# Optimization experiments

Measured on AMD Instinct MI355X. Metric: run time of the kernel, lower is better.

Reference implementation:

```python
import jax, jax.numpy as jnp
import numpy as np

B, NQ, NKV, D = 2, 2048, 2048, 1024
N_HEADS = 16
D_H = D // N_HEADS


def setup_inputs() -> dict:
    key = jax.random.key(0)
    ks = jax.random.split(key, 10)
    s = 0.02  # weight init scale
    return {
        "q": jax.random.normal(ks[0], (B, NQ, D), jnp.float32),
        "kv": jax.random.normal(ks[1], (B, NKV, D), jnp.float32),
        "Wq": jax.random.normal(ks[2], (D, D), jnp.float32) * s,
        "bq": jnp.zeros((D,), jnp.float32),
        "Wk": jax.random.normal(ks[3], (D, D), jnp.float32) * s,
        "bk": jnp.zeros((D,), jnp.float32),
        "Wv": jax.random.normal(ks[4], (D, D), jnp.float32) * s,
        "bv": jnp.zeros((D,), jnp.float32),
        "Wo": jax.random.normal(ks[5], (D, D), jnp.float32) * s,
        "bo": jnp.zeros((D,), jnp.float32),
    }


def reference(q, kv, Wq, bq, Wk, bk, Wv, bv, Wo, bo):
    # Linear projections (torch Linear: x @ W.T + b)
    qh = q @ Wq.T + bq   # [B, NQ, D]
    kh = kv @ Wk.T + bk  # [B, NKV, D]
    vh = kv @ Wv.T + bv  # [B, NKV, D]
    # Split heads: [B, N, H, d_h]
    qh = qh.reshape(B, NQ, N_HEADS, D_H)
    kh = kh.reshape(B, NKV, N_HEADS, D_H)
    vh = vh.reshape(B, NKV, N_HEADS, D_H)
    scale = 1.0 / jnp.sqrt(jnp.asarray(D_H, qh.dtype))
    # QK^T per head: [B, H, NQ, NKV]
    scores = jnp.einsum("bqhd,bkhd->bhqk", qh, kh) * scale
    att = jax.nn.softmax(scores, axis=-1)
    # dropout p=0.0 -> identity
    out = jnp.einsum("bhqk,bkhd->bqhd", att, vh)  # [B, NQ, H, d_h]
    out = out.reshape(B, NQ, D)
    return out @ Wo.T + bo
```

## Files before the change

kernel.cpp:

```cpp
#include <hip/hip_runtime.h>
#include <cstddef>
#include <cstdint>

using half4v  = __attribute__((ext_vector_type(4))) _Float16;
using half8   = __attribute__((ext_vector_type(8))) _Float16;
using floatx4 = __attribute__((ext_vector_type(4))) float;

#define B_   2
#define NQ_  2048
#define DM   1024
#define NH_  16
#define DH_  64
#define NTILES 32

__device__ __forceinline__ void async16(const _Float16* g, _Float16* l) {
    __builtin_amdgcn_global_load_lds(
        (const __attribute__((address_space(1))) unsigned int*)g,
        (__attribute__((address_space(3))) unsigned int*)l, 16, 0, 0);
}

__global__ __launch_bounds__(256) void cvt_all(
        const float* __restrict__ q,  const float* __restrict__ kv,
        const float* __restrict__ wq, const float* __restrict__ wk,
        const float* __restrict__ wv, const float* __restrict__ wo,
        _Float16* __restrict__ dq,  _Float16* __restrict__ dkv,
        _Float16* __restrict__ dwq, _Float16* __restrict__ dwk,
        _Float16* __restrict__ dwv, _Float16* __restrict__ dwo) {
    int blk = blockIdx.x;
    const float* s;
    _Float16* d;
    int base;
    if (blk < 2048)      { s = q;  d = dq;  base = blk; }
    else if (blk < 4096) { s = kv; d = dkv; base = blk - 2048; }
    else if (blk < 4608) { s = wq; d = dwq; base = blk - 4096; }
    else if (blk < 5120) { s = wk; d = dwk; base = blk - 4608; }
    else if (blk < 5632) { s = wv; d = dwv; base = blk - 5120; }
    else                 { s = wo; d = dwo; base = blk - 5632; }
    int i = base * 256 + threadIdx.x;
    const float4* s4 = (const float4*)s;
    float4 a = s4[2 * i], b = s4[2 * i + 1];
    half8 h;
    h[0] = (_Float16)a.x; h[1] = (_Float16)a.y; h[2] = (_Float16)a.z; h[3] = (_Float16)a.w;
    h[4] = (_Float16)b.x; h[5] = (_Float16)b.y; h[6] = (_Float16)b.z; h[7] = (_Float16)b.w;
    ((half8*)d)[i] = h;
}

__global__ __launch_bounds__(256, 3) void proj_qkv(
        const _Float16* __restrict__ q16, const _Float16* __restrict__ kv16,
        const _Float16* __restrict__ wqp, const _Float16* __restrict__ wkp,
        const _Float16* __restrict__ wvp,
        const float* __restrict__ bqp, const float* __restrict__ bkp,
        const float* __restrict__ bvp,
        _Float16* __restrict__ qh, _Float16* __restrict__ kh,
        _Float16* __restrict__ vt) {
    __shared__ _Float16 As[128 * 64];
    __shared__ _Float16 Bs[128 * 64];

    const int which = blockIdx.x >> 8;
    const int sub = blockIdx.x & 255;
    const _Float16* A = (which == 0) ? q16 : kv16;
    const _Float16* W = (which == 0) ? wqp : (which == 1) ? wkp : wvp;
    const float* bias = (which == 0) ? bqp : (which == 1) ? bkp : bvp;

    const int t = threadIdx.x;
    const int w = t >> 6, lane = t & 63;
    const int r16 = lane & 15, quad = lane >> 4;
    const int bm = (sub & 7) * 4 + ((sub >> 3) & 3);
    const int bn = sub >> 5;
    const int m0 = bm * 128, n0 = bn * 128;
    const int wm = w >> 1, wn = w & 1;

    floatx4 acc[4][4];
#pragma unroll
    for (int i = 0; i < 4; i++)
#pragma unroll
        for (int j = 0; j < 4; j++)
#pragma unroll
            for (int r = 0; r < 4; r++) acc[i][j][r] = 0.f;

    const int ph0 = quad ^ (r16 & 7), ph1 = ph0 ^ 4;

    for (int k0 = 0; k0 < DM; k0 += 64) {
        __syncthreads();
#pragma unroll
        for (int i = 0; i < 4; i++) {
            int P = i * 256 + t;
            int m = P >> 3, c = (P & 7) ^ (m & 7);
            async16(A + (size_t)(m0 + m) * DM + k0 + c * 8, &As[P * 8]);
            async16(W + (size_t)(n0 + m) * DM + k0 + c * 8, &Bs[P * 8]);
        }
        asm volatile("s_waitcnt vmcnt(0)" ::: "memory");
        __syncthreads();

        half8 af[4][2], bf[4][2];
#pragma unroll
        for (int mi = 0; mi < 4; mi++) {
            int m = wm * 64 + mi * 16 + r16;
            af[mi][0] = ((const half8*)As)[m * 8 + ph0];
            af[mi][1] = ((const half8*)As)[m * 8 + ph1];
        }
#pragma unroll
        for (int ni = 0; ni < 4; ni++) {
            int n = wn * 64 + ni * 16 + r16;
            bf[ni][0] = ((const half8*)Bs)[n * 8 + ph0];
            bf[ni][1] = ((const half8*)Bs)[n * 8 + ph1];
        }
#pragma unroll
        for (int kd = 0; kd < 2; kd++)
#pragma unroll
            for (int mi = 0; mi < 4; mi++)
#pragma unroll
                for (int ni = 0; ni < 4; ni++)
                    acc[mi][ni] = __builtin_amdgcn_mfma_f32_16x16x32_f16(
                        af[mi][kd], bf[ni][kd], acc[mi][ni], 0, 0, 0);
    }

    if (which < 2) {
        _Float16* C = (which == 0) ? qh : kh;
        const float esc = (which == 0) ? 0.125f : 1.0f;
#pragma unroll
        for (int mi = 0; mi < 4; mi++)
#pragma unroll
            for (int r = 0; r < 4; r++) {
                int row = m0 + wm * 64 + mi * 16 + quad * 4 + r;
#pragma unroll
                for (int ni = 0; ni < 4; ni++) {
                    int col = n0 + wn * 64 + ni * 16 + r16;
                    C[(size_t)row * DM + col] = (_Float16)((acc[mi][ni][r] + bias[col]) * esc);
                }
            }
    } else {
#pragma unroll
        for (int mi = 0; mi < 4; mi++) {
            int krow = m0 + wm * 64 + mi * 16 + quad * 4;
            int bb = krow >> 11, kk = krow & 2047;
#pragma unroll
            for (int ni = 0; ni < 4; ni++) {
                int col = n0 + wn * 64 + ni * 16 + r16;
                int hh = col >> 6, dd = col & 63;
                float bv = bias[col];
                half4v pk;
#pragma unroll
                for (int r = 0; r < 4; r++) pk[r] = (_Float16)(acc[mi][ni][r] + bv);
                *(half4v*)&vt[((size_t)((bb * NH_ + hh) * DH_ + dd)) * NQ_ + kk] = pk;
            }
        }
    }
}

__global__ __launch_bounds__(256, 4) void attn_mfma(const _Float16* __restrict__ Qg,
                                                    const _Float16* __restrict__ Kg,
                                                    const _Float16* __restrict__ Vt,
                                                    _Float16* __restrict__ Og) {
    __shared__ _Float16 Ps[64 * 64];
    __shared__ _Float16 Ks[2][64 * 64];
    __shared__ _Float16 Vs[2][64 * 64];

    const int t = threadIdx.x, w = t >> 6, lane = t & 63;
    const int r16 = lane & 15, quad = lane >> 4;
    const int blk = blockIdx.x;
    const int bh = (blk & 7) * 4 + ((blk >> 3) & 3);
    const int qt = blk >> 5;
    const int b = bh >> 4, h = bh & 15;

    const _Float16* qbase = Qg + (size_t)(b * NQ_ + qt * 64) * DM + h * DH_;
    const _Float16* kbase = Kg + (size_t)(b * NQ_) * DM + h * DH_;
    const _Float16* vbase = Vt + (size_t)bh * DH_ * NQ_;

#pragma unroll
    for (int i = 0; i < 2; i++) {
        int P = i * 256 + t;
        int m = P >> 3, c = (P & 7) ^ (m & 7);
        async16(qbase + (size_t)m * DM + c * 8, &Ps[P * 8]);
        async16(kbase + (size_t)m * DM + c * 8, &Ks[0][P * 8]);
        async16(vbase + (size_t)m * NQ_ + c * 8, &Vs[0][P * 8]);
    }
    asm volatile("s_waitcnt vmcnt(0)" ::: "memory");
    __syncthreads();

    const int ph0 = quad ^ (r16 & 7), ph1 = ph0 ^ 4;
    half8 Qf[2];
    {
        int m = w * 16 + r16;
        Qf[0] = ((const half8*)Ps)[m * 8 + ph0];
        Qf[1] = ((const half8*)Ps)[m * 8 + ph1];
    }

    floatx4 oaccT[4];
    float lacc = 0.f;
#pragma unroll
    for (int nd = 0; nd < 4; nd++)
#pragma unroll
        for (int r = 0; r < 4; r++) oaccT[nd][r] = 0.f;

    for (int kt = 0; kt < NTILES; kt++) {
        const int cur = kt & 1;
        asm volatile("s_waitcnt vmcnt(0)" ::: "memory");
        __syncthreads();

        if (kt + 1 < NTILES) {
            const int nxt = cur ^ 1;
#pragma unroll
            for (int i = 0; i < 2; i++) {
                int P = i * 256 + t;
                int m = P >> 3, c = (P & 7) ^ (m & 7);
                async16(kbase + (size_t)((kt + 1) * 64 + m) * DM + c * 8, &Ks[nxt][P * 8]);
                async16(vbase + (size_t)m * NQ_ + (kt + 1) * 64 + c * 8, &Vs[nxt][P * 8]);
            }
        }

        floatx4 sacc[4];
#pragma unroll
        for (int nk = 0; nk < 4; nk++)
#pragma unroll
            for (int r = 0; r < 4; r++) sacc[nk][r] = 0.f;
#pragma unroll
        for (int kd = 0; kd < 2; kd++)
#pragma unroll
            for (int nk = 0; nk < 4; nk++) {
                half8 kf = ((const half8*)Ks[cur])[(nk * 16 + r16) * 8 + (kd ? ph1 : ph0)];
                sacc[nk] = __builtin_amdgcn_mfma_f32_16x16x32_f16(kf, Qf[kd], sacc[nk], 0, 0, 0);
            }

        const int q = w * 16 + r16;
#pragma unroll
        for (int nk = 0; nk < 4; nk++) {
            float p0 = __expf(sacc[nk][0]);
            float p1 = __expf(sacc[nk][1]);
            float p2 = __expf(sacc[nk][2]);
            float p3 = __expf(sacc[nk][3]);
            lacc += (p0 + p1) + (p2 + p3);
            half4v pk;
            pk[0] = (_Float16)p0; pk[1] = (_Float16)p1;
            pk[2] = (_Float16)p2; pk[3] = (_Float16)p3;
            int phys = (nk * 2 + (quad >> 1)) ^ (r16 & 7);
            *(half4v*)&Ps[q * 64 + phys * 8 + (quad & 1) * 4] = pk;
        }

#pragma unroll
        for (int ks = 0; ks < 2; ks++) {
            half8 pf = ((const half8*)Ps)[q * 8 + ((ks * 4 + quad) ^ (r16 & 7))];
#pragma unroll
            for (int nd = 0; nd < 4; nd++) {
                half8 vf = ((const half8*)Vs[cur])[(nd * 16 + r16) * 8 + ((ks * 4 + quad) ^ (r16 & 7))];
                oaccT[nd] = __builtin_amdgcn_mfma_f32_16x16x32_f16(vf, pf, oaccT[nd], 0, 0, 0);
            }
        }
    }

    {
        float l = lacc;
        l += __shfl_xor(l, 16);
        l += __shfl_xor(l, 32);
        float inv = 1.f / l;
        int qrow = b * NQ_ + qt * 64 + w * 16 + r16;
#pragma unroll
        for (int nd = 0; nd < 4; nd++) {
            half4v o;
#pragma unroll
            for (int r = 0; r < 4; r++) o[r] = (_Float16)(oaccT[nd][r] * inv);
            *(half4v*)&Og[(size_t)qrow * DM + h * DH_ + nd * 16 + quad * 4] = o;
        }
    }
}

__global__ __launch_bounds__(256, 4) void gemm_o(const _Float16* __restrict__ A,
                                                 const _Float16* __restrict__ W,
                                                 const float* __restrict__ bias,
                                                 float* __restrict__ C) {
    __shared__ _Float16 As[64 * 64];
    __shared__ _Float16 Bs[64 * 64];

    const int t = threadIdx.x;
    const int w = t >> 6, lane = t & 63;
    const int r16 = lane & 15, quad = lane >> 4;
    const int blk = blockIdx.x;
    const int bm = (blk & 7) * 8 + ((blk >> 3) & 7);
    const int bn = blk >> 6;
    const int m0 = bm * 64, n0 = bn * 64;
    const int wm = w >> 1, wn = w & 1;

    floatx4 acc[2][2];
#pragma unroll
    for (int i = 0; i < 2; i++)
#pragma unroll
        for (int j = 0; j < 2; j++)
#pragma unroll
            for (int r = 0; r < 4; r++) acc[i][j][r] = 0.f;

    const int ph0 = quad ^ (r16 & 7), ph1 = ph0 ^ 4;

    for (int k0 = 0; k0 < DM; k0 += 64) {
        __syncthreads();
#pragma unroll
        for (int i = 0; i < 2; i++) {
            int P = i * 256 + t;
            int m = P >> 3, c = (P & 7) ^ (m & 7);
            async16(A + (size_t)(m0 + m) * DM + k0 + c * 8, &As[P * 8]);
            async16(W + (size_t)(n0 + m) * DM + k0 + c * 8, &Bs[P * 8]);
        }
        asm volatile("s_waitcnt vmcnt(0)" ::: "memory");
        __syncthreads();

        half8 af[2][2], bf[2][2];
#pragma unroll
        for (int mi = 0; mi < 2; mi++) {
            int m = wm * 32 + mi * 16 + r16;
            af[mi][0] = ((const half8*)As)[m * 8 + ph0];
            af[mi][1] = ((const half8*)As)[m * 8 + ph1];
        }
#pragma unroll
        for (int ni = 0; ni < 2; ni++) {
            int n = wn * 32 + ni * 16 + r16;
            bf[ni][0] = ((const half8*)Bs)[n * 8 + ph0];
            bf[ni][1] = ((const half8*)Bs)[n * 8 + ph1];
        }
#pragma unroll
        for (int kd = 0; kd < 2; kd++)
#pragma unroll
            for (int mi = 0; mi < 2; mi++)
#pragma unroll
                for (int ni = 0; ni < 2; ni++)
                    acc[mi][ni] = __builtin_amdgcn_mfma_f32_16x16x32_f16(
                        af[mi][kd], bf[ni][kd], acc[mi][ni], 0, 0, 0);
    }

#pragma unroll
    for (int mi = 0; mi < 2; mi++)
#pragma unroll
        for (int r = 0; r < 4; r++) {
            int row = m0 + wm * 32 + mi * 16 + quad * 4 + r;
#pragma unroll
            for (int ni = 0; ni < 2; ni++) {
                int col = n0 + wn * 32 + ni * 16 + r16;
                C[(size_t)row * DM + col] = acc[mi][ni][r] + bias[col];
            }
        }
}

extern "C" void kernel_launch(void* const* d_in, const int* in_sizes, int n_in,
                              void* d_out, int out_size, void* d_ws, size_t ws_size,
                              hipStream_t stream) {
    const float* q  = (const float*)d_in[0];
    const float* kv = (const float*)d_in[1];
    const float* Wq = (const float*)d_in[2];
    const float* bq = (const float*)d_in[3];
    const float* Wk = (const float*)d_in[4];
    const float* bk = (const float*)d_in[5];
    const float* Wv = (const float*)d_in[6];
    const float* bv = (const float*)d_in[7];
    const float* Wo = (const float*)d_in[8];
    const float* bo = (const float*)d_in[9];

    char* ws = (char*)d_ws;
    _Float16* q16  = (_Float16*)(ws);
    _Float16* kv16 = (_Float16*)(ws + (size_t)(8  << 20));
    _Float16* w16q = (_Float16*)(ws + (size_t)(16 << 20));
    _Float16* w16k = (_Float16*)(ws + (size_t)(18 << 20));
    _Float16* w16v = (_Float16*)(ws + (size_t)(20 << 20));
    _Float16* w16o = (_Float16*)(ws + (size_t)(22 << 20));
    _Float16* qh16 = (_Float16*)(ws + (size_t)(24 << 20));
    _Float16* kh16 = (_Float16*)(ws + (size_t)(32 << 20));
    _Float16* vt16 = (_Float16*)(ws + (size_t)(40 << 20));
    _Float16* ao16 = (_Float16*)(ws + (size_t)(48 << 20));

    cvt_all<<<6144, 256, 0, stream>>>(q, kv, Wq, Wk, Wv, Wo,
                                      q16, kv16, w16q, w16k, w16v, w16o);

    proj_qkv<<<768, 256, 0, stream>>>(q16, kv16, w16q, w16k, w16v,
                                      bq, bk, bv, qh16, kh16, vt16);

    attn_mfma<<<1024, 256, 0, stream>>>(qh16, kh16, vt16, ao16);

    gemm_o<<<1024, 256, 0, stream>>>(ao16, w16o, bo, (float*)d_out);
}
```

Baseline: 200.5 us.

## Rework attention to 32x32x16 MFMA with 128-row Q tiles and register-resident P

The attention kernel now gives each block 128 query rows instead of 64, so every K/V tile loaded into LDS feeds twice as many queries, and the grid is halved. Matrix ops move from 16x16x32 to 32x32x16 MFMA. The probability tile is handed to the PV product through lane shuffles instead of an LDS write/read, and s_setprio brackets the MFMA sections. In exchange, per-thread register use rises (two 16-wide output accumulators plus a 16-wide score accumulator), which may lower occupancy, and the smaller grid gives fewer blocks to hide latency.

Result: no change. 199.6 us (-0.4%).

```diff
diff --git a/kernel.cpp b/kernel.cpp
--- a/kernel.cpp
+++ b/kernel.cpp
@@ -2,9 +2,10 @@
 #include <cstddef>
 #include <cstdint>
 
-using half4v  = __attribute__((ext_vector_type(4))) _Float16;
-using half8   = __attribute__((ext_vector_type(8))) _Float16;
-using floatx4 = __attribute__((ext_vector_type(4))) float;
+using half4v   = __attribute__((ext_vector_type(4))) _Float16;
+using half8    = __attribute__((ext_vector_type(8))) _Float16;
+using floatx4  = __attribute__((ext_vector_type(4))) float;
+using floatx16 = __attribute__((ext_vector_type(16))) float;
 
 #define B_   2
 #define NQ_  2048
@@ -17,6 +18,12 @@
     __builtin_amdgcn_global_load_lds(
         (const __attribute__((address_space(1))) unsigned int*)g,
         (__attribute__((address_space(3))) unsigned int*)l, 16, 0, 0);
+}
+
+__device__ __forceinline__ unsigned pkh(float a, float b) {
+    union { _Float16 h[2]; unsigned u; } x;
+    x.h[0] = (_Float16)a; x.h[1] = (_Float16)b;
+    return x.u;
 }
 
 __global__ __launch_bounds__(256) void cvt_all(
@@ -152,46 +159,49 @@
                                                     const _Float16* __restrict__ Kg,
                                                     const _Float16* __restrict__ Vt,
                                                     _Float16* __restrict__ Og) {
-    __shared__ _Float16 Ps[64 * 64];
+    __shared__ _Float16 Qs[128 * 64];
     __shared__ _Float16 Ks[2][64 * 64];
     __shared__ _Float16 Vs[2][64 * 64];
 
     const int t = threadIdx.x, w = t >> 6, lane = t & 63;
-    const int r16 = lane & 15, quad = lane >> 4;
+    const int l31 = lane & 31, hi = lane >> 5;
     const int blk = blockIdx.x;
     const int bh = (blk & 7) * 4 + ((blk >> 3) & 3);
     const int qt = blk >> 5;
     const int b = bh >> 4, h = bh & 15;
 
-    const _Float16* qbase = Qg + (size_t)(b * NQ_ + qt * 64) * DM + h * DH_;
+    const _Float16* qbase = Qg + (size_t)(b * NQ_ + qt * 128) * DM + h * DH_;
     const _Float16* kbase = Kg + (size_t)(b * NQ_) * DM + h * DH_;
     const _Float16* vbase = Vt + (size_t)bh * DH_ * NQ_;
 
 #pragma unroll
-    for (int i = 0; i < 2; i++) {
-        int P = i * 256 + t;
+    for (int r = 0; r < 4; r++) {
+        int P = r * 256 + t;
         int m = P >> 3, c = (P & 7) ^ (m & 7);
-        async16(qbase + (size_t)m * DM + c * 8, &Ps[P * 8]);
+        async16(qbase + (size_t)m * DM + c * 8, &Qs[P * 8]);
+    }
+#pragma unroll
+    for (int r = 0; r < 2; r++) {
+        int P = r * 256 + t;
+        int m = P >> 3, c = (P & 7) ^ (m & 7);
         async16(kbase + (size_t)m * DM + c * 8, &Ks[0][P * 8]);
         async16(vbase + (size_t)m * NQ_ + c * 8, &Vs[0][P * 8]);
     }
     asm volatile("s_waitcnt vmcnt(0)" ::: "memory");
     __syncthreads();
 
-    const int ph0 = quad ^ (r16 & 7), ph1 = ph0 ^ 4;
-    half8 Qf[2];
+    half8 qf[4];
     {
-        int m = w * 16 + r16;
-        Qf[0] = ((const half8*)Ps)[m * 8 + ph0];
-        Qf[1] = ((const half8*)Ps)[m * 8 + ph1];
-    }
-
-    floatx4 oaccT[4];
+        int qr = w * 32 + l31;
+#pragma unroll
+        for (int s = 0; s < 4; s++)
+            qf[s] = ((const half8*)Qs)[qr * 8 + ((s * 2 + hi) ^ (qr & 7))];
+    }
+
+    floatx16 oacc0, oacc1;
+#pragma unroll
+    for (int r = 0; r < 16; r++) { oacc0[r] = 0.f; oacc1[r] = 0.f; }
     float lacc = 0.f;
-#pragma unroll
-    for (int nd = 0; nd < 4; nd++)
-#pragma unroll
-        for (int r = 0; r < 4; r++) oaccT[nd][r] = 0.f;
 
     for (int kt = 0; kt < NTILES; kt++) {
         const int cur = kt & 1;
@@ -201,65 +211,88 @@
         if (kt + 1 < NTILES) {
             const int nxt = cur ^ 1;
 #pragma unroll
-            for (int i = 0; i < 2; i++) {
-                int P = i * 256 + t;
+            for (int r = 0; r < 2; r++) {
+                int P = r * 256 + t;
                 int m = P >> 3, c = (P & 7) ^ (m & 7);
                 async16(kbase + (size_t)((kt + 1) * 64 + m) * DM + c * 8, &Ks[nxt][P * 8]);
                 async16(vbase + (size_t)m * NQ_ + (kt + 1) * 64 + c * 8, &Vs[nxt][P * 8]);
             }
         }
 
-        floatx4 sacc[4];
-#pragma unroll
-        for (int nk = 0; nk < 4; nk++)
-#pragma unroll
-            for (int r = 0; r < 4; r++) sacc[nk][r] = 0.f;
-#pragma unroll
-        for (int kd = 0; kd < 2; kd++)
-#pragma unroll
-            for (int nk = 0; nk < 4; nk++) {
-                half8 kf = ((const half8*)Ks[cur])[(nk * 16 + r16) * 8 + (kd ? ph1 : ph0)];
-                sacc[nk] = __builtin_amdgcn_mfma_f32_16x16x32_f16(kf, Qf[kd], sacc[nk], 0, 0, 0);
-            }
-
-        const int q = w * 16 + r16;
-#pragma unroll
-        for (int nk = 0; nk < 4; nk++) {
-            float p0 = __expf(sacc[nk][0]);
-            float p1 = __expf(sacc[nk][1]);
-            float p2 = __expf(sacc[nk][2]);
-            float p3 = __expf(sacc[nk][3]);
-            lacc += (p0 + p1) + (p2 + p3);
-            half4v pk;
-            pk[0] = (_Float16)p0; pk[1] = (_Float16)p1;
-            pk[2] = (_Float16)p2; pk[3] = (_Float16)p3;
-            int phys = (nk * 2 + (quad >> 1)) ^ (r16 & 7);
-            *(half4v*)&Ps[q * 64 + phys * 8 + (quad & 1) * 4] = pk;
-        }
-
-#pragma unroll
-        for (int ks = 0; ks < 2; ks++) {
-            half8 pf = ((const half8*)Ps)[q * 8 + ((ks * 4 + quad) ^ (r16 & 7))];
-#pragma unroll
-            for (int nd = 0; nd < 4; nd++) {
-                half8 vf = ((const half8*)Vs[cur])[(nd * 16 + r16) * 8 + ((ks * 4 + quad) ^ (r16 & 7))];
-                oaccT[nd] = __builtin_amdgcn_mfma_f32_16x16x32_f16(vf, pf, oaccT[nd], 0, 0, 0);
-            }
+#pragma unroll
+        for (int kh2 = 0; kh2 < 2; kh2++) {
+            floatx16 sacc;
+#pragma unroll
+            for (int r = 0; r < 16; r++) sacc[r] = 0.f;
+            __builtin_amdgcn_s_setprio(1);
+#pragma unroll
+            for (int s = 0; s < 4; s++) {
+                half8 kf = ((const half8*)Ks[cur])[(kh2 * 32 + l31) * 8 + ((s * 2 + hi) ^ (l31 & 7))];
+                sacc = __builtin_amdgcn_mfma_f32_32x32x16_f16(kf, qf[s], sacc, 0, 0, 0);
+            }
+            __builtin_amdgcn_s_setprio(0);
+
+#pragma unroll
+            for (int r = 0; r < 16; r++) sacc[r] = __expf(sacc[r]);
+#pragma unroll
+            for (int r = 0; r < 16; r++) lacc += sacc[r];
+
+            half8 pf0, pf1;
+            {
+                unsigned a0 = pkh(sacc[0], sacc[1]),  a1 = pkh(sacc[2], sacc[3]);
+                unsigned b0 = pkh(sacc[4], sacc[5]),  b1 = pkh(sacc[6], sacc[7]);
+                unsigned s0 = hi ? a0 : b0, s1 = hi ? a1 : b1;
+                unsigned r0 = (unsigned)__shfl_xor((int)s0, 32);
+                unsigned r1 = (unsigned)__shfl_xor((int)s1, 32);
+                union { unsigned u[4]; half8 hh; } pu;
+                pu.u[0] = hi ? r0 : a0; pu.u[1] = hi ? r1 : a1;
+                pu.u[2] = hi ? b0 : r0; pu.u[3] = hi ? b1 : r1;
+                pf0 = pu.hh;
+            }
+            {
+                unsigned a0 = pkh(sacc[8], sacc[9]),   a1 = pkh(sacc[10], sacc[11]);
+                unsigned b0 = pkh(sacc[12], sacc[13]), b1 = pkh(sacc[14], sacc[15]);
+                unsigned s0 = hi ? a0 : b0, s1 = hi ? a1 : b1;
+                unsigned r0 = (unsigned)__shfl_xor((int)s0, 32);
+                unsigned r1 = (unsigned)__shfl_xor((int)s1, 32);
+                union { unsigned u[4]; half8 hh; } pu;
+                pu.u[0] = hi ? r0 : a0; pu.u[1] = hi ? r1 : a1;
+                pu.u[2] = hi ? b0 : r0; pu.u[3] = hi ? b1 : r1;
+                pf1 = pu.hh;
+            }
+
+            __builtin_amdgcn_s_setprio(1);
+#pragma unroll
+            for (int s2 = 0; s2 < 2; s2++) {
+                half8 pfk = s2 ? pf1 : pf0;
+                {
+                    half8 vf = ((const half8*)Vs[cur])[(0 * 32 + l31) * 8 + ((kh2 * 4 + s2 * 2 + hi) ^ (l31 & 7))];
+                    oacc0 = __builtin_amdgcn_mfma_f32_32x32x16_f16(vf, pfk, oacc0, 0, 0, 0);
+                }
+                {
+                    half8 vf = ((const half8*)Vs[cur])[(1 * 32 + l31) * 8 + ((kh2 * 4 + s2 * 2 + hi) ^ (l31 & 7))];
+                    oacc1 = __builtin_amdgcn_mfma_f32_32x32x16_f16(vf, pfk, oacc1, 0, 0, 0);
+                }
+            }
+            __builtin_amdgcn_s_setprio(0);
         }
     }
 
     {
-        float l = lacc;
-        l += __shfl_xor(l, 16);
-        l += __shfl_xor(l, 32);
-        float inv = 1.f / l;
-        int qrow = b * NQ_ + qt * 64 + w * 16 + r16;
-#pragma unroll
-        for (int nd = 0; nd < 4; nd++) {
-            half4v o;
-#pragma unroll
-            for (int r = 0; r < 4; r++) o[r] = (_Float16)(oaccT[nd][r] * inv);
-            *(half4v*)&Og[(size_t)qrow * DM + h * DH_ + nd * 16 + quad * 4] = o;
+        float lt = lacc + __shfl_xor(lacc, 32);
+        float linv = 1.f / lt;
+        int qrow = b * NQ_ + qt * 128 + w * 32 + l31;
+#pragma unroll
+        for (int g = 0; g < 4; g++) {
+            half4v o0, o1;
+#pragma unroll
+            for (int j = 0; j < 4; j++) {
+                o0[j] = (_Float16)(oacc0[g * 4 + j] * linv);
+                o1[j] = (_Float16)(oacc1[g * 4 + j] * linv);
+            }
+            int d0 = g * 8 + 4 * hi;
+            *(half4v*)&Og[(size_t)qrow * DM + h * DH_ + d0] = o0;
+            *(half4v*)&Og[(size_t)qrow * DM + h * DH_ + 32 + d0] = o1;
         }
     }
 }
@@ -370,7 +403,7 @@
     proj_qkv<<<768, 256, 0, stream>>>(q16, kv16, w16q, w16k, w16v,
                                       bq, bk, bv, qh16, kh16, vt16);
 
-    attn_mfma<<<1024, 256, 0, stream>>>(qh16, kh16, vt16, ao16);
+    attn_mfma<<<512, 256, 0, stream>>>(qh16, kh16, vt16, ao16);
 
     gemm_o<<<1024, 256, 0, stream>>>(ao16, w16o, bo, (float*)d_out);
 }
```
